# Kernel optimization log

Measured on AMD Instinct MI355X. Metric: run time of the kernel, lower is better.

## Reference

```python
import jax, jax.numpy as jnp
import numpy as np

N_NODES = 50000
N_EDGES = 600000
D_IN = 128
D_OUT = 128


def setup_inputs() -> dict:
    key = jax.random.key(0)
    ks = jax.random.split(key, 10)
    x = jax.random.normal(ks[0], (N_NODES, D_IN), dtype=jnp.float32)
    # glorot init for per-support weights
    scale = jnp.sqrt(6.0 / (D_IN + D_OUT)).astype(jnp.float32)
    W0 = jax.random.uniform(ks[1], (D_IN, D_OUT), dtype=jnp.float32, minval=-scale, maxval=scale)
    W1 = jax.random.uniform(ks[2], (D_IN, D_OUT), dtype=jnp.float32, minval=-scale, maxval=scale)
    b = jnp.zeros((D_OUT,), dtype=jnp.float32)
    rows0 = jax.random.randint(ks[3], (N_EDGES,), 0, N_NODES, dtype=jnp.int32)
    cols0 = jax.random.randint(ks[4], (N_EDGES,), 0, N_NODES, dtype=jnp.int32)
    vals0 = jax.random.uniform(ks[5], (N_EDGES,), dtype=jnp.float32)
    rows1 = jax.random.randint(ks[6], (N_EDGES,), 0, N_NODES, dtype=jnp.int32)
    cols1 = jax.random.randint(ks[7], (N_EDGES,), 0, N_NODES, dtype=jnp.int32)
    vals1 = jax.random.uniform(ks[8], (N_EDGES,), dtype=jnp.float32)
    return {"x": x, "W0": W0, "W1": W1, "b": b,
            "rows0": rows0, "cols0": cols0, "vals0": vals0,
            "rows1": rows1, "cols1": cols1, "vals1": vals1}


def _spmm(rows, cols, vals, dense, num_rows):
    # sparse (COO) x dense: out[r] = sum_e vals[e] * dense[cols[e]] for rows[e]==r
    gathered = vals[:, None] * dense[cols]  # [E, D]
    return jax.ops.segment_sum(gathered, rows, num_segments=num_rows)


def reference(x, W0, W1, b, rows0, cols0, vals0, rows1, cols1, vals1):
    # support 0: A0 @ (x @ W0); support 1: A1 @ (x @ W1); sum, +bias, relu
    pre0 = x @ W0  # [N, D_OUT]
    pre1 = x @ W1
    s0 = _spmm(rows0, cols0, vals0, pre0, N_NODES)
    s1 = _spmm(rows1, cols1, vals1, pre1, N_NODES)
    out = s0 + s1 + b
    return jax.nn.relu(out)
```

## Files before the change

kernel.cpp:

```cpp
#include <hip/hip_runtime.h>

#define N_NODES 50000
#define N_EDGES 600000
#define D 128
#define SB 98
#define NSEG (2 * SB)
#define HISTBLK 2048
#define BINBLK 4096
#define HIST_BLOCKS ((N_EDGES + HISTBLK - 1) / HISTBLK)
#define BIN_BLOCKS ((N_EDGES + BINBLK - 1) / BINBLK)
#define GEMM_BLOCKS ((N_NODES + 63) / 64)
#define SPMM_BLOCKS 2048
#define SPMM_WAVES (SPMM_BLOCKS * 4)

typedef __attribute__((ext_vector_type(8))) short short8v;
typedef __attribute__((ext_vector_type(4))) float f32x4;

__device__ __forceinline__ unsigned short f2bf(float f) {
  unsigned u = __float_as_uint(f);
  return (unsigned short)((u + 0x7FFFu + ((u >> 16) & 1u)) >> 16);
}

__global__ __launch_bounds__(256) void histpack_kernel(
    const int* __restrict__ rows0, const int* __restrict__ rows1,
    int* __restrict__ cnt, const float* __restrict__ W0,
    const float* __restrict__ W1, unsigned short* __restrict__ wpack) {
  const int t = threadIdx.x;
  if (blockIdx.x >= HIST_BLOCKS) {
    const int idx =
        ((blockIdx.x - HIST_BLOCKS) + 8 * blockIdx.y) * 256 + t;
    const int sup = idx >> 11;
    const int ct = (idx >> 8) & 7;
    const int ks = (idx >> 6) & 3;
    const int l = idx & 63;
    const int q = l >> 4;
    const int c = l & 15;
    const float* W = (sup == 0) ? W0 : W1;
    const int d = ct * 16 + c;
    unsigned short v[8];
#pragma unroll
    for (int i = 0; i < 8; ++i) {
      const int k = ks * 32 + q * 8 + i;
      v[i] = f2bf(W[k * D + d]);
    }
    *(uint4*)(wpack + (size_t)idx * 8) = *(uint4*)v;
    return;
  }
  __shared__ int h[SB];
  if (t < SB) h[t] = 0;
  __syncthreads();
  const int sup = blockIdx.y;
  const int* rows = sup ? rows1 : rows0;
  int e = blockIdx.x * HISTBLK + t;
#pragma unroll
  for (int k = 0; k < HISTBLK / 256; ++k, e += 256)
    if (e < N_EDGES) atomicAdd(&h[rows[e] >> 9], 1);
  __syncthreads();
  if (t < SB && h[t] > 0) atomicAdd(&cnt[sup * SB + t], h[t]);
}

__global__ __launch_bounds__(64) void scan196_kernel(
    const int* __restrict__ cnt, int* __restrict__ fillc,
    int* __restrict__ sbstart) {
  const int t = threadIdx.x;
  int v[4];
  int ssum = 0;
#pragma unroll
  for (int k = 0; k < 4; ++k) {
    const int g = t * 4 + k;
    v[k] = (g < NSEG) ? cnt[g] : 0;
    ssum += v[k];
  }
  int run = ssum;
#pragma unroll
  for (int off = 1; off < 64; off <<= 1) {
    const int u = __shfl_up(run, off);
    if (t >= off) run += u;
  }
  int excl = run - ssum;
#pragma unroll
  for (int k = 0; k < 4; ++k) {
    const int g = t * 4 + k;
    if (g < NSEG) {
      fillc[g] = excl;
      sbstart[g] = excl;
    }
    excl += v[k];
  }
  if (t == 63) sbstart[NSEG] = 2 * N_EDGES;
}

union BinGemmSmem {
  struct {
    int hist[SB];
    int lstart[SB];
    int lpos[SB];
    int gbase[SB];
    int2 stage[BINBLK];
  } bin;
  unsigned short sbuf[64][136];
};

__global__ __launch_bounds__(256) void bingemm_kernel(
    const int* __restrict__ rows0, const int* __restrict__ cols0,
    const float* __restrict__ vals0, const int* __restrict__ rows1,
    const int* __restrict__ cols1, const float* __restrict__ vals1,
    int* __restrict__ fillc, int2* __restrict__ cv,
    const float* __restrict__ x, const unsigned short* __restrict__ wpack,
    unsigned short* __restrict__ preb) {
  __shared__ BinGemmSmem sm;
  const int t = threadIdx.x;
  const int bx = blockIdx.x;

  if (bx >= 2 * BIN_BLOCKS) {
    const int gb = bx - 2 * BIN_BLOCKS;
    const int w = t >> 6;
    const int lane = t & 63;
    const int q = lane >> 4;
    const int c = lane & 15;
    const int rowbase = gb * 64;
    const int arow = rowbase + w * 16 + c;

    short8v afrag[4];
#pragma unroll
    for (int ks = 0; ks < 4; ++ks) {
      const int k0 = ks * 32 + q * 8;
      float4 u0 = make_float4(0.f, 0.f, 0.f, 0.f);
      float4 u1 = u0;
      if (arow < N_NODES) {
        u0 = *(const float4*)(x + (size_t)arow * D + k0);
        u1 = *(const float4*)(x + (size_t)arow * D + k0 + 4);
      }
      unsigned short a[8];
      a[0] = f2bf(u0.x); a[1] = f2bf(u0.y);
      a[2] = f2bf(u0.z); a[3] = f2bf(u0.w);
      a[4] = f2bf(u1.x); a[5] = f2bf(u1.y);
      a[6] = f2bf(u1.z); a[7] = f2bf(u1.w);
      afrag[ks] = *(const short8v*)a;
    }

    const short8v* wp = (const short8v*)wpack;
#pragma unroll
    for (int sup = 0; sup < 2; ++sup) {
      unsigned short* pb = preb + (size_t)sup * N_NODES * D;
#pragma unroll
      for (int ct = 0; ct < 8; ++ct) {
        f32x4 acc = {0.f, 0.f, 0.f, 0.f};
#pragma unroll
        for (int ks = 0; ks < 4; ++ks) {
          const short8v bfrag = wp[((sup * 8 + ct) * 4 + ks) * 64 + lane];
          acc = __builtin_amdgcn_mfma_f32_16x16x32_bf16(afrag[ks], bfrag, acc,
                                                        0, 0, 0);
        }
#pragma unroll
        for (int j = 0; j < 4; ++j)
          sm.sbuf[w * 16 + q * 4 + j][ct * 16 + c] = f2bf(acc[j]);
      }
      __syncthreads();
#pragma unroll
      for (int it = 0; it < 4; ++it) {
        const int idx = t + it * 256;
        const int row = idx >> 4;
        const int dseg = (idx & 15) * 8;
        const uint4 v = *(const uint4*)&sm.sbuf[row][dseg];
        const int grow = rowbase + row;
        if (grow < N_NODES) *(uint4*)(pb + (size_t)grow * D + dseg) = v;
      }
      __syncthreads();
    }
    return;
  }

  const int sup = (bx >= BIN_BLOCKS) ? 1 : 0;
  const int bb = bx - sup * BIN_BLOCKS;
  const int* rows = sup ? rows1 : rows0;
  const int* cols = sup ? cols1 : cols0;
  const float* vals = sup ? vals1 : vals0;
  const int ebase = bb * BINBLK;
  const int nloc = min(BINBLK, N_EDGES - ebase);

  if (t < SB) sm.bin.hist[t] = 0;
  __syncthreads();

  int myr[16], myc[16];
  float myv[16];
#pragma unroll
  for (int k = 0; k < 16; ++k) {
    const int i = t + k * 256;
    myr[k] = -1;
    if (i < nloc) {
      myr[k] = rows[ebase + i];
      myc[k] = cols[ebase + i];
      myv[k] = vals[ebase + i];
      atomicAdd(&sm.bin.hist[myr[k] >> 9], 1);
    }
  }
  __syncthreads();

  if (t < 64) {
    const int g0 = 2 * t, g1 = 2 * t + 1;
    const int v0 = (g0 < SB) ? sm.bin.hist[g0] : 0;
    const int v1 = (g1 < SB) ? sm.bin.hist[g1] : 0;
    const int ssum = v0 + v1;
    int run = ssum;
#pragma unroll
    for (int off = 1; off < 64; off <<= 1) {
      const int u = __shfl_up(run, off);
      if (t >= off) run += u;
    }
    const int excl = run - ssum;
    if (g0 < SB) {
      sm.bin.lstart[g0] = excl;
      sm.bin.lpos[g0] = excl;
    }
    if (g1 < SB) {
      sm.bin.lstart[g1] = excl + v0;
      sm.bin.lpos[g1] = excl + v0;
    }
  }
  __syncthreads();

#pragma unroll
  for (int k = 0; k < 16; ++k) {
    if (myr[k] >= 0) {
      const int sb = myr[k] >> 9;
      const int p = atomicAdd(&sm.bin.lpos[sb], 1);
      sm.bin.stage[p] =
          make_int2(myc[k] | ((myr[k] & 511) << 16) | (sb << 25),
                    __float_as_int(myv[k]));
    }
  }
  if (t < SB && sm.bin.hist[t] > 0)
    sm.bin.gbase[t] = atomicAdd(&fillc[sup * SB + t], sm.bin.hist[t]);
  __syncthreads();

  for (int i = t; i < nloc; i += 256) {
    const int2 ev = sm.bin.stage[i];
    const int sb = ((unsigned)ev.x) >> 25;
    cv[sm.bin.gbase[sb] + (i - sm.bin.lstart[sb])] = ev;
  }
}

__global__ __launch_bounds__(1024) void sort_kernel(
    const int* __restrict__ sbstart, int2* __restrict__ cv,
    int* __restrict__ rs) {
  const int sb = blockIdx.x;
  const int sup = blockIdx.y;
  const int s = sbstart[sup * SB + sb];
  const int e = sbstart[sup * SB + sb + 1];
  const int n = e - s;
  const int t = threadIdx.x;

  __shared__ int cnt[512];
  __shared__ int base[512];
  __shared__ int off[512];
  if (t < 512) {
    cnt[t] = 0;
    off[t] = 0;
  }
  __syncthreads();

  int2 ed[8];
#pragma unroll
  for (int k = 0; k < 8; ++k) {
    const int i = t + k * 1024;
    if (i < n) {
      ed[k] = cv[s + i];
      atomicAdd(&cnt[(ed[k].x >> 16) & 511], 1);
    }
  }
  __syncthreads();

  if (t < 64) {
    int v[8];
    int ssum = 0;
#pragma unroll
    for (int k = 0; k < 8; ++k) {
      v[k] = cnt[t * 8 + k];
      ssum += v[k];
    }
    int run = ssum;
#pragma unroll
    for (int off2 = 1; off2 < 64; off2 <<= 1) {
      const int u = __shfl_up(run, off2);
      if (t >= off2) run += u;
    }
    int excl = run - ssum;
#pragma unroll
    for (int k = 0; k < 8; ++k) {
      base[t * 8 + k] = excl;
      excl += v[k];
    }
  }
  __syncthreads();

  if (t < 512) {
    const int row = sb * 512 + t;
    if (row < N_NODES) rs[sup * (N_NODES + 1) + row] = s + base[t];
  }
  if (sb == SB - 1 && t == 0) rs[sup * (N_NODES + 1) + N_NODES] = e;

#pragma unroll
  for (int k = 0; k < 8; ++k) {
    const int i = t + k * 1024;
    if (i < n) {
      const int rl = (ed[k].x >> 16) & 511;
      const int pos = base[rl] + atomicAdd(&off[rl], 1);
      cv[s + pos] = ed[k];
    }
  }
}

__global__ __launch_bounds__(256) void spmm_fused_kernel(
    const int* __restrict__ rs, const int2* __restrict__ cv,
    const unsigned short* __restrict__ preb, const float* __restrict__ bias,
    float* __restrict__ out) {
  const int lane = threadIdx.x & 63;
  const int g = lane >> 4;
  const int dbase = (lane & 15) << 3;
  const int wid = blockIdx.x * 4 + (threadIdx.x >> 6);

  const float4 b0 = *(const float4*)(bias + dbase);
  const float4 b1 = *(const float4*)(bias + dbase + 4);

  for (int row = wid; row < N_NODES; row += SPMM_WAVES) {
    float acc[8];
#pragma unroll
    for (int i = 0; i < 8; ++i) acc[i] = 0.f;

#pragma unroll
    for (int sup = 0; sup < 2; ++sup) {
      const int s = rs[sup * (N_NODES + 1) + row];
      const int e = rs[sup * (N_NODES + 1) + row + 1];
      const unsigned short* pb = preb + (size_t)sup * N_NODES * D;
      int j = s + g;
      for (; j + 4 < e; j += 8) {
        const int2 e0 = cv[j];
        const int2 e1 = cv[j + 4];
        const uint4 q0 = *(const uint4*)(pb + (size_t)(e0.x & 0xFFFF) * D + dbase);
        const uint4 q1 = *(const uint4*)(pb + (size_t)(e1.x & 0xFFFF) * D + dbase);
        const float v0 = __int_as_float(e0.y);
        const float v1 = __int_as_float(e1.y);
        acc[0] = fmaf(v0, __uint_as_float(q0.x << 16), acc[0]);
        acc[1] = fmaf(v0, __uint_as_float(q0.x & 0xFFFF0000u), acc[1]);
        acc[2] = fmaf(v0, __uint_as_float(q0.y << 16), acc[2]);
        acc[3] = fmaf(v0, __uint_as_float(q0.y & 0xFFFF0000u), acc[3]);
        acc[4] = fmaf(v0, __uint_as_float(q0.z << 16), acc[4]);
        acc[5] = fmaf(v0, __uint_as_float(q0.z & 0xFFFF0000u), acc[5]);
        acc[6] = fmaf(v0, __uint_as_float(q0.w << 16), acc[6]);
        acc[7] = fmaf(v0, __uint_as_float(q0.w & 0xFFFF0000u), acc[7]);
        acc[0] = fmaf(v1, __uint_as_float(q1.x << 16), acc[0]);
        acc[1] = fmaf(v1, __uint_as_float(q1.x & 0xFFFF0000u), acc[1]);
        acc[2] = fmaf(v1, __uint_as_float(q1.y << 16), acc[2]);
        acc[3] = fmaf(v1, __uint_as_float(q1.y & 0xFFFF0000u), acc[3]);
        acc[4] = fmaf(v1, __uint_as_float(q1.z << 16), acc[4]);
        acc[5] = fmaf(v1, __uint_as_float(q1.z & 0xFFFF0000u), acc[5]);
        acc[6] = fmaf(v1, __uint_as_float(q1.w << 16), acc[6]);
        acc[7] = fmaf(v1, __uint_as_float(q1.w & 0xFFFF0000u), acc[7]);
      }
      if (j < e) {
        const int2 e0 = cv[j];
        const uint4 q0 = *(const uint4*)(pb + (size_t)(e0.x & 0xFFFF) * D + dbase);
        const float v0 = __int_as_float(e0.y);
        acc[0] = fmaf(v0, __uint_as_float(q0.x << 16), acc[0]);
        acc[1] = fmaf(v0, __uint_as_float(q0.x & 0xFFFF0000u), acc[1]);
        acc[2] = fmaf(v0, __uint_as_float(q0.y << 16), acc[2]);
        acc[3] = fmaf(v0, __uint_as_float(q0.y & 0xFFFF0000u), acc[3]);
        acc[4] = fmaf(v0, __uint_as_float(q0.z << 16), acc[4]);
        acc[5] = fmaf(v0, __uint_as_float(q0.z & 0xFFFF0000u), acc[5]);
        acc[6] = fmaf(v0, __uint_as_float(q0.w << 16), acc[6]);
        acc[7] = fmaf(v0, __uint_as_float(q0.w & 0xFFFF0000u), acc[7]);
      }
    }

#pragma unroll
    for (int i = 0; i < 8; ++i) {
      acc[i] += __shfl_xor(acc[i], 16);
      acc[i] += __shfl_xor(acc[i], 32);
    }

    if (g == 0) {
      float4 r0, r1;
      r0.x = fmaxf(acc[0] + b0.x, 0.f);
      r0.y = fmaxf(acc[1] + b0.y, 0.f);
      r0.z = fmaxf(acc[2] + b0.z, 0.f);
      r0.w = fmaxf(acc[3] + b0.w, 0.f);
      r1.x = fmaxf(acc[4] + b1.x, 0.f);
      r1.y = fmaxf(acc[5] + b1.y, 0.f);
      r1.z = fmaxf(acc[6] + b1.z, 0.f);
      r1.w = fmaxf(acc[7] + b1.w, 0.f);
      float* op = out + (size_t)row * D + dbase;
      *(float4*)op = r0;
      *(float4*)(op + 4) = r1;
    }
  }
}

__global__ __launch_bounds__(256) void gemm_f32_kernel(
    const float* __restrict__ x, const float* __restrict__ W,
    float* __restrict__ pre) {
  const int tid = threadIdx.x;
  const int nloc = (tid >> 5) << 3;
  const int d4 = (tid & 31) << 2;
  const int nbase = blockIdx.x * 64;
  __shared__ float xs[64][D];
  {
    float4* xs4 = (float4*)(&xs[0][0]);
    const float4* xg4 = (const float4*)x;
#pragma unroll
    for (int i = 0; i < 8; ++i) {
      const int idx = tid + i * 256;
      const int row = nbase + (idx >> 5);
      xs4[idx] = (row < N_NODES) ? xg4[(size_t)row * 32 + (idx & 31)]
                                 : make_float4(0.f, 0.f, 0.f, 0.f);
    }
  }
  __syncthreads();
  float4 acc[8];
#pragma unroll
  for (int i = 0; i < 8; ++i) acc[i] = make_float4(0.f, 0.f, 0.f, 0.f);
  for (int k = 0; k < D; ++k) {
    const float4 w = *(const float4*)(W + k * D + d4);
#pragma unroll
    for (int i = 0; i < 8; ++i) {
      const float xv = xs[nloc + i][k];
      acc[i].x = fmaf(xv, w.x, acc[i].x);
      acc[i].y = fmaf(xv, w.y, acc[i].y);
      acc[i].z = fmaf(xv, w.z, acc[i].z);
      acc[i].w = fmaf(xv, w.w, acc[i].w);
    }
  }
#pragma unroll
  for (int i = 0; i < 8; ++i) {
    const int n = nbase + nloc + i;
    if (n < N_NODES) *(float4*)(pre + (size_t)n * D + d4) = acc[i];
  }
}

__global__ __launch_bounds__(256) void spmm_scatter_kernel(
    const int* __restrict__ rows, const int* __restrict__ cols,
    const float* __restrict__ vals, const float* __restrict__ pre,
    float* __restrict__ out) {
  const long long idx = (long long)blockIdx.x * blockDim.x + threadIdx.x;
  const int e = (int)(idx >> 6);
  if (e >= N_EDGES) return;
  const int dd = ((int)idx & 63) << 1;
  const int r = rows[e];
  const int c = cols[e];
  const float v = vals[e];
  const float2 p = *(const float2*)(pre + (size_t)c * D + dd);
  float* outp = out + (size_t)r * D + dd;
  atomicAdd(outp + 0, v * p.x);
  atomicAdd(outp + 1, v * p.y);
}

__global__ __launch_bounds__(256) void bias_relu_kernel(
    float* __restrict__ out, const float* __restrict__ b) {
  const int idx = blockIdx.x * blockDim.x + threadIdx.x;
  float4 v = ((float4*)out)[idx];
  const float4 bb = ((const float4*)b)[idx & 31];
  v.x = fmaxf(v.x + bb.x, 0.f);
  v.y = fmaxf(v.y + bb.y, 0.f);
  v.z = fmaxf(v.z + bb.z, 0.f);
  v.w = fmaxf(v.w + bb.w, 0.f);
  ((float4*)out)[idx] = v;
}

extern "C" void kernel_launch(void* const* d_in, const int* in_sizes, int n_in,
                              void* d_out, int out_size, void* d_ws,
                              size_t ws_size, hipStream_t stream) {
  const float* x = (const float*)d_in[0];
  const float* W0 = (const float*)d_in[1];
  const float* W1 = (const float*)d_in[2];
  const float* b = (const float*)d_in[3];
  const int* rows0 = (const int*)d_in[4];
  const int* cols0 = (const int*)d_in[5];
  const float* vals0 = (const float*)d_in[6];
  const int* rows1 = (const int*)d_in[7];
  const int* cols1 = (const int*)d_in[8];
  const float* vals1 = (const float*)d_in[9];
  float* out = (float*)d_out;

  auto align_up = [](size_t v) { return (v + 255) & ~(size_t)255; };
  const size_t PREB = align_up((size_t)2 * N_NODES * D * 2);
  const size_t CV = align_up((size_t)2 * N_EDGES * 8);
  const size_t CNT = align_up((size_t)NSEG * 4);
  const size_t FILLC = align_up((size_t)NSEG * 4);
  const size_t SBSTART = align_up((size_t)(NSEG + 1) * 4);
  const size_t RS = align_up((size_t)2 * (N_NODES + 1) * 4);
  const size_t WPACK = align_up((size_t)2 * D * D * 2);
  const size_t NEED = PREB + CV + CNT + FILLC + SBSTART + RS + WPACK;

  char* wsc = (char*)d_ws;

  if (ws_size >= NEED) {
    unsigned short* preb = (unsigned short*)wsc;
    int2* cv = (int2*)(wsc + PREB);
    int* cnt = (int*)(wsc + PREB + CV);
    int* fillc = (int*)(wsc + PREB + CV + CNT);
    int* sbstart = (int*)(wsc + PREB + CV + CNT + FILLC);
    int* rs = (int*)(wsc + PREB + CV + CNT + FILLC + SBSTART);
    unsigned short* wpack =
        (unsigned short*)(wsc + PREB + CV + CNT + FILLC + SBSTART + RS);

    hipMemsetAsync(cnt, 0, (size_t)NSEG * 4, stream);
    histpack_kernel<<<dim3(HIST_BLOCKS + 8, 2), 256, 0, stream>>>(
        rows0, rows1, cnt, W0, W1, wpack);
    scan196_kernel<<<1, 64, 0, stream>>>(cnt, fillc, sbstart);
    bingemm_kernel<<<2 * BIN_BLOCKS + GEMM_BLOCKS, 256, 0, stream>>>(
        rows0, cols0, vals0, rows1, cols1, vals1, fillc, cv, x, wpack, preb);
    sort_kernel<<<dim3(SB, 2), 1024, 0, stream>>>(sbstart, cv, rs);
    spmm_fused_kernel<<<SPMM_BLOCKS, 256, 0, stream>>>(rs, cv, preb, b, out);
  } else {
    float* pre = (float*)wsc;
    hipMemsetAsync(d_out, 0, (size_t)N_NODES * D * 4, stream);
    const int scat_blocks = (N_EDGES * 64 + 255) / 256;
    gemm_f32_kernel<<<GEMM_BLOCKS, 256, 0, stream>>>(x, W0, pre);
    spmm_scatter_kernel<<<scat_blocks, 256, 0, stream>>>(rows0, cols0, vals0,
                                                         pre, out);
    gemm_f32_kernel<<<GEMM_BLOCKS, 256, 0, stream>>>(x, W1, pre);
    spmm_scatter_kernel<<<scat_blocks, 256, 0, stream>>>(rows1, cols1, vals1,
                                                         pre, out);
    bias_relu_kernel<<<(N_NODES * D / 4) / 256, 256, 0, stream>>>(out, b);
  }
}
```

Baseline: 102.8 us.

## Replace histogram+scan pass with fixed-capacity per-segment bins

Edges are now binned into fixed-capacity slots (CAP entries per super-block segment), which removes the histogram kernel, the scan kernel and the memset. A small init kernel packs weights and zeroes the fill counters. The sort kernel reads segment counts from the fill counters and writes separate row start and end arrays, since rows are no longer contiguous across segments. This cuts two launches and one full pass over the row indices. In exchange it assumes no segment exceeds CAP edges, which holds for uniform random rows (about 6100 expected per segment) but would overflow on skewed inputs.

```diff
diff --git a/kernel.cpp b/kernel.cpp
--- a/kernel.cpp
+++ b/kernel.cpp
@@ -5,6 +5,7 @@
 #define D 128
 #define SB 98
 #define NSEG (2 * SB)
+#define CAP 8192
 #define HISTBLK 2048
 #define BINBLK 4096
 #define HIST_BLOCKS ((N_EDGES + HISTBLK - 1) / HISTBLK)
@@ -21,29 +22,45 @@
   return (unsigned short)((u + 0x7FFFu + ((u >> 16) & 1u)) >> 16);
 }
 
+__device__ __forceinline__ void wpack_one(int idx, const float* __restrict__ W0,
+                                          const float* __restrict__ W1,
+                                          unsigned short* __restrict__ wpack) {
+  const int sup = idx >> 11;
+  const int ct = (idx >> 8) & 7;
+  const int ks = (idx >> 6) & 3;
+  const int l = idx & 63;
+  const int q = l >> 4;
+  const int c = l & 15;
+  const float* W = (sup == 0) ? W0 : W1;
+  const int d = ct * 16 + c;
+  unsigned short v[8];
+#pragma unroll
+  for (int i = 0; i < 8; ++i) {
+    const int k = ks * 32 + q * 8 + i;
+    v[i] = f2bf(W[k * D + d]);
+  }
+  *(uint4*)(wpack + (size_t)idx * 8) = *(uint4*)v;
+}
+
+__global__ __launch_bounds__(256) void init_kernel(
+    const float* __restrict__ W0, const float* __restrict__ W1,
+    unsigned short* __restrict__ wpack, int* __restrict__ fillc) {
+  const int t = threadIdx.x;
+  if (blockIdx.x == 16) {
+    if (t < NSEG) fillc[t] = 0;
+    return;
+  }
+  wpack_one(blockIdx.x * 256 + t, W0, W1, wpack);
+}
+
 __global__ __launch_bounds__(256) void histpack_kernel(
     const int* __restrict__ rows0, const int* __restrict__ rows1,
     int* __restrict__ cnt, const float* __restrict__ W0,
     const float* __restrict__ W1, unsigned short* __restrict__ wpack) {
   const int t = threadIdx.x;
   if (blockIdx.x >= HIST_BLOCKS) {
-    const int idx =
-        ((blockIdx.x - HIST_BLOCKS) + 8 * blockIdx.y) * 256 + t;
-    const int sup = idx >> 11;
-    const int ct = (idx >> 8) & 7;
-    const int ks = (idx >> 6) & 3;
-    const int l = idx & 63;
-    const int q = l >> 4;
-    const int c = l & 15;
-    const float* W = (sup == 0) ? W0 : W1;
-    const int d = ct * 16 + c;
-    unsigned short v[8];
-#pragma unroll
-    for (int i = 0; i < 8; ++i) {
-      const int k = ks * 32 + q * 8 + i;
-      v[i] = f2bf(W[k * D + d]);
-    }
-    *(uint4*)(wpack + (size_t)idx * 8) = *(uint4*)v;
+    wpack_one(((blockIdx.x - HIST_BLOCKS) + 8 * blockIdx.y) * 256 + t, W0, W1,
+              wpack);
     return;
   }
   __shared__ int h[SB];
@@ -101,6 +118,7 @@
   unsigned short sbuf[64][136];
 };
 
+template <bool CAPPED>
 __global__ __launch_bounds__(256) void bingemm_kernel(
     const int* __restrict__ rows0, const int* __restrict__ cols0,
     const float* __restrict__ vals0, const int* __restrict__ rows1,
@@ -230,8 +248,11 @@
                     __float_as_int(myv[k]));
     }
   }
-  if (t < SB && sm.bin.hist[t] > 0)
-    sm.bin.gbase[t] = atomicAdd(&fillc[sup * SB + t], sm.bin.hist[t]);
+  if (t < SB && sm.bin.hist[t] > 0) {
+    const int seg = sup * SB + t;
+    const int bump = atomicAdd(&fillc[seg], sm.bin.hist[t]);
+    sm.bin.gbase[t] = (CAPPED ? seg * CAP : 0) + bump;
+  }
   __syncthreads();
 
   for (int i = t; i < nloc; i += 256) {
@@ -241,14 +262,15 @@
   }
 }
 
+template <bool CAPPED>
 __global__ __launch_bounds__(1024) void sort_kernel(
-    const int* __restrict__ sbstart, int2* __restrict__ cv,
-    int* __restrict__ rs) {
+    const int* __restrict__ sbstart, const int* __restrict__ fillc,
+    int2* __restrict__ cv, int* __restrict__ rs_s, int* __restrict__ rs_e) {
   const int sb = blockIdx.x;
   const int sup = blockIdx.y;
-  const int s = sbstart[sup * SB + sb];
-  const int e = sbstart[sup * SB + sb + 1];
-  const int n = e - s;
+  const int seg = sup * SB + sb;
+  const int s = CAPPED ? seg * CAP : sbstart[seg];
+  const int n = CAPPED ? fillc[seg] : (sbstart[seg + 1] - s);
   const int t = threadIdx.x;
 
   __shared__ int cnt[512];
@@ -296,9 +318,11 @@
 
   if (t < 512) {
     const int row = sb * 512 + t;
-    if (row < N_NODES) rs[sup * (N_NODES + 1) + row] = s + base[t];
-  }
-  if (sb == SB - 1 && t == 0) rs[sup * (N_NODES + 1) + N_NODES] = e;
+    if (row < N_NODES) {
+      rs_s[sup * N_NODES + row] = s + base[t];
+      rs_e[sup * N_NODES + row] = s + base[t] + cnt[t];
+    }
+  }
 
 #pragma unroll
   for (int k = 0; k < 8; ++k) {
@@ -312,9 +336,9 @@
 }
 
 __global__ __launch_bounds__(256) void spmm_fused_kernel(
-    const int* __restrict__ rs, const int2* __restrict__ cv,
-    const unsigned short* __restrict__ preb, const float* __restrict__ bias,
-    float* __restrict__ out) {
+    const int* __restrict__ rs_s, const int* __restrict__ rs_e,
+    const int2* __restrict__ cv, const unsigned short* __restrict__ preb,
+    const float* __restrict__ bias, float* __restrict__ out) {
   const int lane = threadIdx.x & 63;
   const int g = lane >> 4;
   const int dbase = (lane & 15) << 3;
@@ -330,8 +354,8 @@
 
 #pragma unroll
     for (int sup = 0; sup < 2; ++sup) {
-      const int s = rs[sup * (N_NODES + 1) + row];
-      const int e = rs[sup * (N_NODES + 1) + row + 1];
+      const int s = rs_s[sup * N_NODES + row];
+      const int e = rs_e[sup * N_NODES + row];
       const unsigned short* pb = preb + (size_t)sup * N_NODES * D;
       int j = s + g;
       for (; j + 4 < e; j += 8) {
@@ -483,34 +507,56 @@
 
   auto align_up = [](size_t v) { return (v + 255) & ~(size_t)255; };
   const size_t PREB = align_up((size_t)2 * N_NODES * D * 2);
+  const size_t FILLC = align_up((size_t)NSEG * 4);
+  const size_t RS1 = align_up((size_t)2 * N_NODES * 4);
+  const size_t WPACK = align_up((size_t)2 * D * D * 2);
+
+  const size_t CVC = align_up((size_t)NSEG * CAP * 8);
+  const size_t NEED_A = PREB + CVC + FILLC + 2 * RS1 + WPACK;
   const size_t CV = align_up((size_t)2 * N_EDGES * 8);
   const size_t CNT = align_up((size_t)NSEG * 4);
-  const size_t FILLC = align_up((size_t)NSEG * 4);
   const size_t SBSTART = align_up((size_t)(NSEG + 1) * 4);
-  const size_t RS = align_up((size_t)2 * (N_NODES + 1) * 4);
-  const size_t WPACK = align_up((size_t)2 * D * D * 2);
-  const size_t NEED = PREB + CV + CNT + FILLC + SBSTART + RS + WPACK;
+  const size_t NEED_B = PREB + CV + CNT + FILLC + SBSTART + 2 * RS1 + WPACK;
 
   char* wsc = (char*)d_ws;
 
-  if (ws_size >= NEED) {
+  if (ws_size >= NEED_A) {
+    unsigned short* preb = (unsigned short*)wsc;
+    int2* cv = (int2*)(wsc + PREB);
+    int* fillc = (int*)(wsc + PREB + CVC);
+    int* rs_s = (int*)(wsc + PREB + CVC + FILLC);
+    int* rs_e = (int*)(wsc + PREB + CVC + FILLC + RS1);
+    unsigned short* wpack =
+        (unsigned short*)(wsc + PREB + CVC + FILLC + 2 * RS1);
+
+    init_kernel<<<17, 256, 0, stream>>>(W0, W1, wpack, fillc);
+    bingemm_kernel<true><<<2 * BIN_BLOCKS + GEMM_BLOCKS, 256, 0, stream>>>(
+        rows0, cols0, vals0, rows1, cols1, vals1, fillc, cv, x, wpack, preb);
+    sort_kernel<true><<<dim3(SB, 2), 1024, 0, stream>>>(nullptr, fillc, cv,
+                                                        rs_s, rs_e);
+    spmm_fused_kernel<<<SPMM_BLOCKS, 256, 0, stream>>>(rs_s, rs_e, cv, preb, b,
+                                                       out);
+  } else if (ws_size >= NEED_B) {
     unsigned short* preb = (unsigned short*)wsc;
     int2* cv = (int2*)(wsc + PREB);
     int* cnt = (int*)(wsc + PREB + CV);
     int* fillc = (int*)(wsc + PREB + CV + CNT);
     int* sbstart = (int*)(wsc + PREB + CV + CNT + FILLC);
-    int* rs = (int*)(wsc + PREB + CV + CNT + FILLC + SBSTART);
+    int* rs_s = (int*)(wsc + PREB + CV + CNT + FILLC + SBSTART);
+    int* rs_e = (int*)(wsc + PREB + CV + CNT + FILLC + SBSTART + RS1);
     unsigned short* wpack =
-        (unsigned short*)(wsc + PREB + CV + CNT + FILLC + SBSTART + RS);
+        (unsigned short*)(wsc + PREB + CV + CNT + FILLC + SBSTART + 2 * RS1);
 
     hipMemsetAsync(cnt, 0, (size_t)NSEG * 4, stream);
     histpack_kernel<<<dim3(HIST_BLOCKS + 8, 2), 256, 0, stream>>>(
         rows0, rows1, cnt, W0, W1, wpack);
     scan196_kernel<<<1, 64, 0, stream>>>(cnt, fillc, sbstart);
-    bingemm_kernel<<<2 * BIN_BLOCKS + GEMM_BLOCKS, 256, 0, stream>>>(
+    bingemm_kernel<false><<<2 * BIN_BLOCKS + GEMM_BLOCKS, 256, 0, stream>>>(
         rows0, cols0, vals0, rows1, cols1, vals1, fillc, cv, x, wpack, preb);
-    sort_kernel<<<dim3(SB, 2), 1024, 0, stream>>>(sbstart, cv, rs);
-    spmm_fused_kernel<<<SPMM_BLOCKS, 256, 0, stream>>>(rs, cv, preb, b, out);
+    sort_kernel<false><<<dim3(SB, 2), 1024, 0, stream>>>(sbstart, nullptr, cv,
+                                                         rs_s, rs_e);
+    spmm_fused_kernel<<<SPMM_BLOCKS, 256, 0, stream>>>(rs_s, rs_e, cv, preb, b,
+                                                       out);
   } else {
     float* pre = (float*)wsc;
     hipMemsetAsync(d_out, 0, (size_t)N_NODES * D * 4, stream);
```

After: 89.14 us. 1.15x faster.
